# Optimization experiments

Measured on AMD Instinct MI355X. Metric: run time of the kernel, lower is better.

The kernel has to match this reference:

```python
import jax, jax.numpy as jnp
import numpy as np

B, N, C = 4, 2048, 768
H = 12
HD = C // H  # 64
SCALE = HD ** -0.5


def setup_inputs() -> dict:
    key = jax.random.key(0)
    ks = jax.random.split(key, 3)
    x = jax.random.normal(ks[0], (B, N, C), dtype=jnp.float32)
    w_qkv = jax.random.normal(ks[1], (C, 3 * C), dtype=jnp.float32) * (C ** -0.5)
    b_qkv = jnp.zeros((3 * C,), dtype=jnp.float32)
    w_proj = jax.random.normal(ks[2], (C, C), dtype=jnp.float32) * (C ** -0.5)
    b_proj = jnp.zeros((C,), dtype=jnp.float32)
    return {"x": x, "w_qkv": w_qkv, "b_qkv": b_qkv, "w_proj": w_proj, "b_proj": b_proj}


def reference(x, w_qkv, b_qkv, w_proj, b_proj):
    # fused QKV projection: [B, N, 3C] -> [3, B, H, N, HD]
    qkv = (x @ w_qkv + b_qkv).reshape(B, N, 3, H, HD).transpose(2, 0, 3, 1, 4)
    q, k, v = qkv[0] * SCALE, qkv[1], qkv[2]
    # scores [B, H, N, N] (Global mixer: no mask)
    attn = jnp.einsum('bhnd,bhmd->bhnm', q, k)
    attn = jax.nn.softmax(attn, axis=-1)
    # attn @ V -> [B, N, C]
    out = jnp.einsum('bhnm,bhmd->bhnd', attn, v).transpose(0, 2, 1, 3).reshape(B, N, C)
    return out @ w_proj + b_proj
```

## Files before the change

kernel.cpp:

```cpp
#include <hip/hip_runtime.h>
#include <hip/hip_bf16.h>
#include <math.h>

#define B_ 4
#define N_ 2048
#define C_ 768
#define H_ 12
#define HD_ 64

typedef short short8 __attribute__((ext_vector_type(8)));
typedef float float16v __attribute__((ext_vector_type(16)));
typedef unsigned short u16;
typedef unsigned int u32;

static __device__ __forceinline__ u16 f2bf(float x) {
    __hip_bfloat16 b = __float2bfloat16(x);
    return *reinterpret_cast<u16*>(&b);
}
#if defined(__has_builtin)
#if __has_builtin(__builtin_amdgcn_exp2f)
#define EXP2F_FAST __builtin_amdgcn_exp2f
#endif
#endif
#ifndef EXP2F_FAST
#define EXP2F_FAST exp2f
#endif
static __device__ __forceinline__ u32 cpk(float lo, float hi) {
    u32 r;
    asm("v_cvt_pk_bf16_f32 %0, %1, %2" : "=v"(r) : "v"(lo), "v"(hi));
    return r;
}
static __device__ __forceinline__ void gload_lds16(const u16* g, u16* l) {
    __builtin_amdgcn_global_load_lds(
        (const __attribute__((address_space(1))) void*)g,
        (__attribute__((address_space(3))) void*)l, 16, 0, 0);
}

__global__ __launch_bounds__(256) void cast_bf16_kernel(
    const float* __restrict__ X, u16* __restrict__ Xb, int n4)
{
    int i = blockIdx.x * 256 + threadIdx.x;
    if (i < n4) {
        float4 v = ((const float4*)X)[i];
        uint2 o = make_uint2(cpk(v.x, v.y), cpk(v.z, v.w));
        ((uint2*)Xb)[i] = o;
    }
}

__global__ __launch_bounds__(256) void transpose_cvt_kernel(
    const float* __restrict__ W, u16* __restrict__ Wt, int R, int Cc)
{
    __shared__ float tile[64][65];
    const int t = threadIdx.x;
    const int r0 = blockIdx.y * 64, c0 = blockIdx.x * 64;
    const int tr = t >> 4, tc = (t & 15) * 4;
#pragma unroll
    for (int i = 0; i < 4; i++) {
        float4 v = *(const float4*)(W + (size_t)(r0 + tr + i * 16) * Cc + c0 + tc);
        tile[tr + i * 16][tc + 0] = v.x;
        tile[tr + i * 16][tc + 1] = v.y;
        tile[tr + i * 16][tc + 2] = v.z;
        tile[tr + i * 16][tc + 3] = v.w;
    }
    __syncthreads();
#pragma unroll
    for (int i = 0; i < 4; i++) {
        int n = tr + i * 16;
        int k = tc;
        uint2 o = make_uint2(cpk(tile[k + 0][n], tile[k + 1][n]),
                             cpk(tile[k + 2][n], tile[k + 3][n]));
        *(uint2*)(Wt + (size_t)(c0 + n) * R + r0 + k) = o;
    }
}

template<int BM, int BN, bool OUT_BF16, bool BIAS_ROW>
__global__ __launch_bounds__(256) void gemm_mfma_kernel(
    const u16* __restrict__ A, int lda,
    const u16* __restrict__ Bt,
    const float* __restrict__ bias,
    void* __restrict__ C, int ldc,
    int K, float scale, int scale_cols)
{
    constexpr int WM = BM / 2, WN = BN / 2;
    constexpr int MR = WM / 32, NR = WN / 32;
    constexpr int SR = (BM + BN) / 4;
    constexpr int NI = SR / 8;

    __shared__ u16 As[BM * 64];
    __shared__ u16 Bs[BN * 64];
    const int t = threadIdx.x;
    const int w = t >> 6, lane = t & 63, ln = lane & 31, e = lane >> 5;
    const int wm = w >> 1, wn = w & 1;
    const int row0 = blockIdx.y * BM, col0 = blockIdx.x * BN;
    const int r_sub = lane >> 3;
    const int cg = (lane & 7) ^ r_sub;

    float16v acc[MR][NR];
#pragma unroll
    for (int sm = 0; sm < MR; sm++)
#pragma unroll
        for (int sn = 0; sn < NR; sn++)
#pragma unroll
            for (int i = 0; i < 16; i++) acc[sm][sn][i] = 0.f;

    for (int k0 = 0; k0 < K; k0 += 64) {
        __syncthreads();
#pragma unroll
        for (int i = 0; i < NI; i++) {
            int g = w * SR + i * 8;
            if (g < BM) {
                const u16* ga = A + (size_t)(row0 + g + r_sub) * lda + k0 + cg * 8;
                gload_lds16(ga, As + g * 64);
            } else {
                int gb_ = g - BM;
                const u16* gb = Bt + (size_t)(col0 + gb_ + r_sub) * K + k0 + cg * 8;
                gload_lds16(gb, Bs + gb_ * 64);
            }
        }
        __syncthreads();

#pragma unroll
        for (int ks = 0; ks < 4; ks++) {
            short8 af[MR], bf[NR];
#pragma unroll
            for (int sm = 0; sm < MR; sm++) {
                int r = wm * WM + sm * 32 + ln;
                af[sm] = *(const short8*)&As[r * 64 + ((2 * ks + e) ^ (r & 7)) * 8];
            }
#pragma unroll
            for (int sn = 0; sn < NR; sn++) {
                int r = wn * WN + sn * 32 + ln;
                bf[sn] = *(const short8*)&Bs[r * 64 + ((2 * ks + e) ^ (r & 7)) * 8];
            }
#pragma unroll
            for (int sm = 0; sm < MR; sm++)
#pragma unroll
                for (int sn = 0; sn < NR; sn++)
                    acc[sm][sn] = __builtin_amdgcn_mfma_f32_32x32x16_bf16(
                        af[sm], bf[sn], acc[sm][sn], 0, 0, 0);
        }
    }

    const float sc = (col0 < scale_cols) ? scale : 1.0f;
#pragma unroll
    for (int sm = 0; sm < MR; sm++)
#pragma unroll
        for (int sn = 0; sn < NR; sn++) {
            int col = col0 + wn * WN + sn * 32 + ln;
            float bvc = BIAS_ROW ? 0.f : bias[col];
#pragma unroll
            for (int reg = 0; reg < 16; reg++) {
                int row = row0 + wm * WM + sm * 32 + (reg & 3) + 8 * (reg >> 2) + 4 * e;
                float bv = BIAS_ROW ? bias[row] : bvc;
                float v = (acc[sm][sn][reg] + bv) * sc;
                if (OUT_BF16)
                    ((u16*)C)[(size_t)row * ldc + col] = f2bf(v);
                else
                    ((float*)C)[(size_t)row * ldc + col] = v;
            }
        }
}

__global__ __launch_bounds__(256) void attn_kernel(
    const u16* __restrict__ qk, const u16* __restrict__ Vt, u16* __restrict__ Ob)
{
    __shared__ __align__(16) u16 lds_us[17664];

    const int t = threadIdx.x;
    const int w = t >> 6, lane = t & 63, ln = lane & 31, e = lane >> 5;
    const int rt = w & 1, kt = w >> 1;
    const int r_sub = lane >> 3;
    const int cgk = (lane & 7) ^ r_sub;

    const int bid = blockIdx.x;
    const int xcd = bid & 7, j = bid >> 3;
    const int bh = xcd * 6 + (j >> 4);
    const int b = bh / H_, h = bh % H_;
    const int row0 = (j & 15) * 128;

    const u16* kq0 = qk + (size_t)b * N_ * 1536 + 768 + h * 64 + cgk * 8
                        + (size_t)(w * 16 + r_sub) * 1536;
    const u16* kq1 = kq0 + (size_t)8 * 1536;
    const u16* vq0 = Vt + (size_t)(h * 64 + w * 16 + r_sub) * (B_ * N_)
                        + b * N_ + cgk * 8;
    const u16* vq1 = vq0 + (size_t)8 * (B_ * N_);

    {
        u16* Kp = lds_us;
        u16* Vp = lds_us + 4096;
        gload_lds16(kq0, Kp + (w * 16 + 0) * 64);
        gload_lds16(kq1, Kp + (w * 16 + 8) * 64);
        gload_lds16(vq0, Vp + (w * 16 + 0) * 64);
        gload_lds16(vq1, Vp + (w * 16 + 8) * 64);
        kq0 += (size_t)64 * 1536; kq1 += (size_t)64 * 1536;
        vq0 += 64; vq1 += 64;
    }

    short8 qfA[4], qfB[4];
    {
        const u16* qa = qk + (size_t)(b * N_ + row0 + rt * 64 + ln) * 1536 + h * 64;
#pragma unroll
        for (int ks = 0; ks < 4; ks++) {
            qfA[ks] = __builtin_bit_cast(short8, *(const uint4*)(qa + ks * 16 + e * 8));
            qfB[ks] = __builtin_bit_cast(short8, *(const uint4*)(qa + 32 * 1536 + ks * 16 + e * 8));
        }
    }

    float16v accA0, accA1, accB0, accB1;
#pragma unroll
    for (int i = 0; i < 16; i++) { accA0[i] = 0.f; accA1[i] = 0.f; accB0[i] = 0.f; accB1[i] = 0.f; }
    float lA = 0.f, lB = 0.f;

    for (int c = 0; c < N_ / 64; c++) {
        __syncthreads();
        if (c + 1 < N_ / 64) {
            u16* Kp = lds_us + ((c + 1) & 1) * 8192;
            u16* Vp = Kp + 4096;
            gload_lds16(kq0, Kp + (w * 16 + 0) * 64);
            gload_lds16(kq1, Kp + (w * 16 + 8) * 64);
            gload_lds16(vq0, Vp + (w * 16 + 0) * 64);
            gload_lds16(vq1, Vp + (w * 16 + 8) * 64);
            kq0 += (size_t)64 * 1536; kq1 += (size_t)64 * 1536;
            vq0 += 64; vq1 += 64;
        }
        const u16* Ks = lds_us + (c & 1) * 8192;
        const u16* Vs = Ks + 4096;

        float16v sA, sB;
#pragma unroll
        for (int i = 0; i < 16; i++) { sA[i] = 0.f; sB[i] = 0.f; }
        const int krow = kt * 32 + ln;
#pragma unroll
        for (int ks = 0; ks < 4; ks++) {
            int slot = (2 * ks + e) ^ (ln & 7);
            short8 kf = *(const short8*)&Ks[krow * 64 + slot * 8];
            sA = __builtin_amdgcn_mfma_f32_32x32x16_bf16(kf, qfA[ks], sA, 0, 0, 0);
            sB = __builtin_amdgcn_mfma_f32_32x32x16_bf16(kf, qfB[ks], sB, 0, 0, 0);
        }

#pragma unroll
        for (int i = 0; i < 16; i++) {
            sA[i] = EXP2F_FAST(sA[i]);
            sB[i] = EXP2F_FAST(sB[i]);
        }
        {
            float a0 = (sA[0] + sA[1]) + (sA[2] + sA[3]);
            float a1 = (sA[4] + sA[5]) + (sA[6] + sA[7]);
            float a2 = (sA[8] + sA[9]) + (sA[10] + sA[11]);
            float a3 = (sA[12] + sA[13]) + (sA[14] + sA[15]);
            float b0 = (sB[0] + sB[1]) + (sB[2] + sB[3]);
            float b1 = (sB[4] + sB[5]) + (sB[6] + sB[7]);
            float b2 = (sB[8] + sB[9]) + (sB[10] + sB[11]);
            float b3 = (sB[12] + sB[13]) + (sB[14] + sB[15]);
            float la = (a0 + a1) + (a2 + a3);
            float lb = (b0 + b1) + (b2 + b3);
            lA += la + __shfl_xor(la, 32);
            lB += lb + __shfl_xor(lb, 32);
        }

#pragma unroll
        for (int g2 = 0; g2 < 2; g2++) {
            uint4 pA4 = make_uint4(cpk(sA[8 * g2 + 0], sA[8 * g2 + 1]),
                                   cpk(sA[8 * g2 + 2], sA[8 * g2 + 3]),
                                   cpk(sA[8 * g2 + 4], sA[8 * g2 + 5]),
                                   cpk(sA[8 * g2 + 6], sA[8 * g2 + 7]));
            uint4 pB4 = make_uint4(cpk(sB[8 * g2 + 0], sB[8 * g2 + 1]),
                                   cpk(sB[8 * g2 + 2], sB[8 * g2 + 3]),
                                   cpk(sB[8 * g2 + 4], sB[8 * g2 + 5]),
                                   cpk(sB[8 * g2 + 6], sB[8 * g2 + 7]));
            short8 pfA = __builtin_bit_cast(short8, pA4);
            short8 pfB = __builtin_bit_cast(short8, pB4);

            const int c0 = 4 * kt + 2 * g2;
#pragma unroll
            for (int dh = 0; dh < 2; dh++) {
                int d = dh * 32 + ln;
                uint2 r1 = *(const uint2*)&Vs[d * 64 + ((c0 ^ (d & 7)) * 8) + 4 * e];
                uint2 r2 = *(const uint2*)&Vs[d * 64 + (((c0 + 1) ^ (d & 7)) * 8) + 4 * e];
                uint4 va4 = make_uint4(r1.x, r1.y, r2.x, r2.y);
                short8 va = __builtin_bit_cast(short8, va4);
                if (dh == 0) {
                    accA0 = __builtin_amdgcn_mfma_f32_32x32x16_bf16(va, pfA, accA0, 0, 0, 0);
                    accB0 = __builtin_amdgcn_mfma_f32_32x32x16_bf16(va, pfB, accB0, 0, 0, 0);
                } else {
                    accA1 = __builtin_amdgcn_mfma_f32_32x32x16_bf16(va, pfA, accA1, 0, 0, 0);
                    accB1 = __builtin_amdgcn_mfma_f32_32x32x16_bf16(va, pfB, accB1, 0, 0, 0);
                }
            }
        }
    }

    __syncthreads();
    float* Osf = (float*)lds_us;
    float* lred = Osf + 128 * 68;
    const int rowA = rt * 64 + ln, rowB = rt * 64 + 32 + ln;

    if (kt == 1) {
#pragma unroll
        for (int reg = 0; reg < 16; reg++) {
            int d = (reg & 3) + 8 * (reg >> 2) + 4 * e;
            Osf[rowA * 68 + d]      = accA0[reg];
            Osf[rowA * 68 + d + 32] = accA1[reg];
            Osf[rowB * 68 + d]      = accB0[reg];
            Osf[rowB * 68 + d + 32] = accB1[reg];
        }
        lred[rowA] = lA;
        lred[rowB] = lB;
    }
    __syncthreads();
    if (kt == 0) {
        float linvA = 1.0f / (lA + lred[rowA]);
        float linvB = 1.0f / (lB + lred[rowB]);
#pragma unroll
        for (int reg = 0; reg < 16; reg++) {
            int d = (reg & 3) + 8 * (reg >> 2) + 4 * e;
            Osf[rowA * 68 + d]      = (accA0[reg] + Osf[rowA * 68 + d]) * linvA;
            Osf[rowA * 68 + d + 32] = (accA1[reg] + Osf[rowA * 68 + d + 32]) * linvA;
            Osf[rowB * 68 + d]      = (accB0[reg] + Osf[rowB * 68 + d]) * linvB;
            Osf[rowB * 68 + d + 32] = (accB1[reg] + Osf[rowB * 68 + d + 32]) * linvB;
        }
#pragma unroll
        for (int j2 = 0; j2 < 8; j2++) {
            int idx = lane + j2 * 64;
            int r = idx >> 3, gg = idx & 7;
            float4 o0 = *(float4*)&Osf[(rt * 64 + r) * 68 + gg * 8];
            float4 o1 = *(float4*)&Osf[(rt * 64 + r) * 68 + gg * 8 + 4];
            uint4 ov = make_uint4(cpk(o0.x, o0.y), cpk(o0.z, o0.w),
                                  cpk(o1.x, o1.y), cpk(o1.z, o1.w));
            *(uint4*)(Ob + (size_t)(b * N_ + row0 + rt * 64 + r) * 768
                         + h * 64 + gg * 8) = ov;
        }
    }
}

extern "C" void kernel_launch(void* const* d_in, const int* in_sizes, int n_in,
                              void* d_out, int out_size, void* d_ws, size_t ws_size,
                              hipStream_t stream) {
    const float* x      = (const float*)d_in[0];
    const float* w_qkv  = (const float*)d_in[1];
    const float* b_qkv  = (const float*)d_in[2];
    const float* w_proj = (const float*)d_in[3];
    const float* b_proj = (const float*)d_in[4];
    float* out = (float*)d_out;

    char* ws = (char*)d_ws;
    u16* qk2    = (u16*)ws;
    u16* Vt     = (u16*)(ws + 25165824);
    u16* Ob     = (u16*)(ws + 37748736);
    u16* xb     = (u16*)(ws + 50331648);
    u16* wqkvT  = (u16*)(ws + 62914560);
    u16* wprojT = (u16*)(ws + 66453504);

    cast_bf16_kernel<<<6144, 256, 0, stream>>>(x, xb, (B_ * N_ * C_) / 4);
    transpose_cvt_kernel<<<dim3(36, 12), 256, 0, stream>>>(w_qkv, wqkvT, C_, 3 * C_);
    transpose_cvt_kernel<<<dim3(12, 12), 256, 0, stream>>>(w_proj, wprojT, C_, C_);

    gemm_mfma_kernel<128, 128, true, false><<<dim3(12, 64), 256, 0, stream>>>(
        xb, C_, wqkvT, b_qkv, qk2, 1536, C_, 0.18033688011112042f, 768);

    gemm_mfma_kernel<64, 128, true, true><<<dim3(64, 12), 256, 0, stream>>>(
        wqkvT + (size_t)1536 * C_, C_, xb, b_qkv + 1536, Vt, B_ * N_, C_, 1.0f, 0);

    attn_kernel<<<768, 256, 0, stream>>>(qk2, Vt, Ob);

    gemm_mfma_kernel<128, 64, false, false><<<dim3(12, 64), 256, 0, stream>>>(
        Ob, C_, wprojT, b_proj, out, C_, C_, 1.0f, 0);
}
```

Measured before the change: 232.4 us.

## Merge QK and V projection GEMMs into one launch; use inline v_exp_f32

Combines the QK projection GEMM and the transposed V projection GEMM into a single kernel that splits on block index. Both branches share one shared-memory buffer sized for the larger tile. This removes one launch and the tail gap between the two GEMMs so their blocks can run concurrently. It also swaps the builtin exp2 for inline v_exp_f32 assembly in the attention softmax, which may block some compiler scheduling. The larger static LDS allocation can lower occupancy for the smaller V-tile blocks.

After: 232.1 us. Within noise of the previous version (-0.1%).

```diff
diff --git a/kernel.cpp b/kernel.cpp
--- a/kernel.cpp
+++ b/kernel.cpp
@@ -17,14 +17,11 @@
     __hip_bfloat16 b = __float2bfloat16(x);
     return *reinterpret_cast<u16*>(&b);
 }
-#if defined(__has_builtin)
-#if __has_builtin(__builtin_amdgcn_exp2f)
-#define EXP2F_FAST __builtin_amdgcn_exp2f
-#endif
-#endif
-#ifndef EXP2F_FAST
-#define EXP2F_FAST exp2f
-#endif
+static __device__ __forceinline__ float exp2_hw(float x) {
+    float r;
+    asm("v_exp_f32 %0, %1" : "=v"(r) : "v"(x));
+    return r;
+}
 static __device__ __forceinline__ u32 cpk(float lo, float hi) {
     u32 r;
     asm("v_cvt_pk_bf16_f32 %0, %1, %2" : "=v"(r) : "v"(lo), "v"(hi));
@@ -74,24 +71,23 @@
 }
 
 template<int BM, int BN, bool OUT_BF16, bool BIAS_ROW>
-__global__ __launch_bounds__(256) void gemm_mfma_kernel(
+static __device__ __forceinline__ void gemm_tile_body(
+    u16* __restrict__ As, u16* __restrict__ Bs,
     const u16* __restrict__ A, int lda,
     const u16* __restrict__ Bt,
     const float* __restrict__ bias,
     void* __restrict__ C, int ldc,
-    int K, float scale, int scale_cols)
+    int K, float scale, int scale_cols, int bx, int by)
 {
     constexpr int WM = BM / 2, WN = BN / 2;
     constexpr int MR = WM / 32, NR = WN / 32;
     constexpr int SR = (BM + BN) / 4;
     constexpr int NI = SR / 8;
 
-    __shared__ u16 As[BM * 64];
-    __shared__ u16 Bs[BN * 64];
     const int t = threadIdx.x;
     const int w = t >> 6, lane = t & 63, ln = lane & 31, e = lane >> 5;
     const int wm = w >> 1, wn = w & 1;
-    const int row0 = blockIdx.y * BM, col0 = blockIdx.x * BN;
+    const int row0 = by * BM, col0 = bx * BN;
     const int r_sub = lane >> 3;
     const int cg = (lane & 7) ^ r_sub;
 
@@ -159,6 +155,42 @@
                     ((float*)C)[(size_t)row * ldc + col] = v;
             }
         }
+}
+
+template<int BM, int BN, bool OUT_BF16, bool BIAS_ROW>
+__global__ __launch_bounds__(256) void gemm_mfma_kernel(
+    const u16* __restrict__ A, int lda,
+    const u16* __restrict__ Bt,
+    const float* __restrict__ bias,
+    void* __restrict__ C, int ldc,
+    int K, float scale, int scale_cols)
+{
+    __shared__ u16 As[BM * 64];
+    __shared__ u16 Bs[BN * 64];
+    gemm_tile_body<BM, BN, OUT_BF16, BIAS_ROW>(
+        As, Bs, A, lda, Bt, bias, C, ldc, K, scale, scale_cols,
+        blockIdx.x, blockIdx.y);
+}
+
+__global__ __launch_bounds__(256) void qkv_gemm_fused_kernel(
+    const u16* __restrict__ xb, const u16* __restrict__ wqkvT,
+    const float* __restrict__ b_qkv,
+    u16* __restrict__ qk2, u16* __restrict__ Vt)
+{
+    __shared__ u16 sh[16384];
+    const int id = blockIdx.x;
+    if (id < 768) {
+        gemm_tile_body<128, 128, true, false>(
+            sh, sh + 128 * 64,
+            xb, C_, wqkvT, b_qkv, qk2, 1536, C_,
+            0.18033688011112042f, 768, id % 12, id / 12);
+    } else {
+        const int id2 = id - 768;
+        gemm_tile_body<64, 128, true, true>(
+            sh, sh + 64 * 64,
+            wqkvT + (size_t)1536 * C_, C_, xb, b_qkv + 1536,
+            Vt, B_ * N_, C_, 1.0f, 0, id2 % 64, id2 / 64);
+    }
 }
 
 __global__ __launch_bounds__(256) void attn_kernel(
@@ -240,8 +272,8 @@
 
 #pragma unroll
         for (int i = 0; i < 16; i++) {
-            sA[i] = EXP2F_FAST(sA[i]);
-            sB[i] = EXP2F_FAST(sB[i]);
+            sA[i] = exp2_hw(sA[i]);
+            sB[i] = exp2_hw(sB[i]);
         }
         {
             float a0 = (sA[0] + sA[1]) + (sA[2] + sA[3]);
@@ -355,11 +387,7 @@
     transpose_cvt_kernel<<<dim3(36, 12), 256, 0, stream>>>(w_qkv, wqkvT, C_, 3 * C_);
     transpose_cvt_kernel<<<dim3(12, 12), 256, 0, stream>>>(w_proj, wprojT, C_, C_);
 
-    gemm_mfma_kernel<128, 128, true, false><<<dim3(12, 64), 256, 0, stream>>>(
-        xb, C_, wqkvT, b_qkv, qk2, 1536, C_, 0.18033688011112042f, 768);
-
-    gemm_mfma_kernel<64, 128, true, true><<<dim3(64, 12), 256, 0, stream>>>(
-        wqkvT + (size_t)1536 * C_, C_, xb, b_qkv + 1536, Vt, B_ * N_, C_, 1.0f, 0);
+    qkv_gemm_fused_kernel<<<1536, 256, 0, stream>>>(xb, wqkvT, b_qkv, qk2, Vt);
 
     attn_kernel<<<768, 256, 0, stream>>>(qk2, Vt, Ob);
 
```
